# Optimization experiments

Measured on AMD Instinct MI355X. Metric: run time of the kernel, lower is better.

## Reference

```python
import jax, jax.numpy as jnp
import numpy as np

S, B, I, H = 512, 64, 1024, 1024


def setup_inputs() -> dict:
    key = jax.random.key(0)
    ks = jax.random.split(key, 17)
    sI = 1.0 / np.sqrt(I)
    sH = 1.0 / np.sqrt(H)
    d = {"x": jax.random.normal(ks[0], (S, B, I), dtype=jnp.float32)}
    names = ["i", "f", "c", "o"]
    for n, g in enumerate(names):
        d[f"w_x{g}"] = jax.random.uniform(ks[1 + 4 * n], (H, I), jnp.float32, -sI, sI)
        d[f"b_x{g}"] = jax.random.uniform(ks[2 + 4 * n], (H,), jnp.float32, -sI, sI)
        d[f"w_h{g}"] = jax.random.uniform(ks[3 + 4 * n], (H, H), jnp.float32, -sH, sH)
        d[f"b_h{g}"] = jax.random.uniform(ks[4 + 4 * n], (H,), jnp.float32, -sH, sH)
        d[f"b_{g}"] = jnp.zeros((H,), jnp.float32)
    return d


def reference(x, w_xi, b_xi, w_hi, b_hi, b_i,
              w_xf, b_xf, w_hf, b_hf, b_f,
              w_xc, b_xc, w_hc, b_hc, b_c,
              w_xo, b_xo, w_ho, b_ho, b_o):
    seq_len, batch, _ = x.shape
    hid = w_hi.shape[0]
    # Precompute all input-side projections in one big GEMM per gate: [S,B,H].
    # Fold the three bias vectors of each gate (b_x*, b_h*, b_*) in here; math
    # is identical to adding them per step.
    gx_i = jnp.einsum('sbi,hi->sbh', x, w_xi) + (b_xi + b_hi + b_i)
    gx_f = jnp.einsum('sbi,hi->sbh', x, w_xf) + (b_xf + b_hf + b_f)
    gx_c = jnp.einsum('sbi,hi->sbh', x, w_xc) + (b_xc + b_hc + b_c)
    gx_o = jnp.einsum('sbi,hi->sbh', x, w_xo) + (b_xo + b_ho + b_o)

    h0 = jnp.zeros((batch, hid), x.dtype)
    c0 = jnp.zeros((batch, hid), x.dtype)

    def step(carry, gx):
        h, c = carry
        xi, xf, xc, xo = gx
        i_t = jax.nn.sigmoid(xi + h @ w_hi.T)
        f_t = jax.nn.sigmoid(xf + h @ w_hf.T)
        g_t = jnp.tanh(xc + h @ w_hc.T)
        o_t = jax.nn.sigmoid(xo + h @ w_ho.T)
        c = f_t * c + i_t * g_t
        h = o_t * jnp.tanh(c)
        return (h, c), h

    (h, c), outputs = jax.lax.scan(step, (h0, c0), (gx_i, gx_f, gx_c, gx_o))
    return outputs, (h, c)
```

## Files before the change

kernel.cpp:

```cpp
#include <hip/hip_runtime.h>
#include <cstdint>
#include <cstddef>

#define S_LEN 512
#define NB    64
#define NI    1024
#define NH    1024
#define NR    4096
#define NGRP  4
#define WPG   64
#define BPG   16
#define HSLOT 33792
#define FLAGSTRIDE 16

typedef short bf16x8 __attribute__((ext_vector_type(8)));
typedef float f32x4  __attribute__((ext_vector_type(4)));

__device__ __forceinline__ short f2bf(float f) {
  uint32_t u = __float_as_uint(f);
  u += 0x7fff + ((u >> 16) & 1);
  return (short)(u >> 16);
}
__device__ __forceinline__ float bf2f(short s) {
  return __uint_as_float(((uint32_t)(uint16_t)s) << 16);
}
__device__ __forceinline__ void gload16(const void* g, void* l) {
  __builtin_amdgcn_global_load_lds((const __attribute__((address_space(1))) void*)g,
                                   (__attribute__((address_space(3))) void*)l, 16, 0, 0);
}
__device__ __forceinline__ float sigm(float x) { return 1.0f / (1.0f + __expf(-x)); }
__device__ __forceinline__ float tanh_fast(float x) {
  return 2.0f / (1.0f + __expf(-2.0f * x)) - 1.0f;
}

__device__ __forceinline__ void astore32(void* p, uint32_t v) {
  __hip_atomic_store((uint32_t*)p, v, __ATOMIC_RELAXED, __HIP_MEMORY_SCOPE_AGENT);
}
__device__ __forceinline__ void astore16(void* p, uint16_t v) {
  __hip_atomic_store((uint16_t*)p, v, __ATOMIC_RELAXED, __HIP_MEMORY_SCOPE_AGENT);
}
__device__ __forceinline__ uint32_t aload32(const void* p) {
  return __hip_atomic_load((const uint32_t*)p, __ATOMIC_RELAXED, __HIP_MEMORY_SCOPE_AGENT);
}


__global__ __launch_bounds__(256) void k_convert_x(const float* __restrict__ x,
                                                   short* __restrict__ xbf) {
  int tid = blockIdx.x * 256 + threadIdx.x;
  float4 v = ((const float4*)x)[tid];
  short4 o;
  o.x = f2bf(v.x); o.y = f2bf(v.y); o.z = f2bf(v.z); o.w = f2bf(v.w);
  ((short4*)xbf)[tid] = o;
}

struct WPtrs { const float *xi, *xf, *xc, *xo, *hi, *hf, *hc, *ho; };

__global__ __launch_bounds__(256) void k_pack_w(WPtrs w, short* __restrict__ wxcat,
                                                short* __restrict__ whcat) {
  int tid  = blockIdx.x * 256 + threadIdx.x;
  int flat = tid * 4;
  int r = flat >> 10, k = flat & 1023;
  int j = r >> 2, g = r & 3;
  const float* px = (g == 0) ? w.xi : (g == 1) ? w.xf : (g == 2) ? w.xc : w.xo;
  const float* ph = (g == 0) ? w.hi : (g == 1) ? w.hf : (g == 2) ? w.hc : w.ho;
  float4 vx = *(const float4*)(px + j * 1024 + k);
  float4 vh = *(const float4*)(ph + j * 1024 + k);
  short4 ox, oh;
  ox.x = f2bf(vx.x); ox.y = f2bf(vx.y); ox.z = f2bf(vx.z); ox.w = f2bf(vx.w);
  oh.x = f2bf(vh.x); oh.y = f2bf(vh.y); oh.z = f2bf(vh.z); oh.w = f2bf(vh.w);
  *(short4*)(wxcat + flat) = ox;
  *(short4*)(whcat + flat) = oh;
}

struct BPtrs { const float *xi,*hi,*i_, *xf,*hf,*f_, *xc,*hc,*c_, *xo,*ho,*o_; };

__global__ __launch_bounds__(256) void k_init(BPtrs p, float* __restrict__ bias,
                                              unsigned int* __restrict__ flags) {
  int tid = blockIdx.x * 256 + threadIdx.x;
  flags[tid] = 0;
  int j = tid >> 2, g = tid & 3;
  const float* bx = (g == 0) ? p.xi : (g == 1) ? p.xf : (g == 2) ? p.xc : p.xo;
  const float* bh = (g == 0) ? p.hi : (g == 1) ? p.hf : (g == 2) ? p.hc : p.ho;
  const float* bb = (g == 0) ? p.i_ : (g == 1) ? p.f_ : (g == 2) ? p.c_ : p.o_;
  bias[tid] = bx[j] + bh[j] + bb[j];
}


__global__ __launch_bounds__(256) void gemm_x(const short* __restrict__ xbf,
                                              const short* __restrict__ wx,
                                              const float* __restrict__ bias,
                                              short* __restrict__ gx) {
  __shared__ __align__(16) short As[2][4096];
  __shared__ __align__(16) short Bs[2][4096];

  const int tid = threadIdx.x, wave = tid >> 6, lane = tid & 63;
  const int m0 = blockIdx.x * 128, n0 = blockIdx.y * 128;
  const char* aB = (const char*)xbf + (size_t)m0 * 2048;
  const char* bB = (const char*)wx + (size_t)n0 * 2048;

  f32x4 acc[4][4] = {};

  auto stage = [&](int kt, int buf) {
#pragma unroll
    for (int s2 = 0; s2 < 2; ++s2) {
      int seg = wave * 2 + s2;
      int L   = seg * 1024 + lane * 16;
      int row = L >> 6;
      int cb  = L & 63;
      gload16(aB + (size_t)row * 2048 + kt * 64 + cb, (char*)&As[buf][0] + L);
      gload16(bB + (size_t)row * 2048 + kt * 64 + cb, (char*)&Bs[buf][0] + L);
    }
  };

  const int wm = wave >> 1, wn = wave & 1;
  auto compute = [&](int buf) {
    const char* Ab = (const char*)&As[buf][0];
    const char* Bb = (const char*)&Bs[buf][0];
    bf16x8 a[4], b[4];
#pragma unroll
    for (int f = 0; f < 4; ++f) {
      int ar = wm * 64 + f * 16 + (lane & 15);
      a[f] = *(const bf16x8*)(Ab + ar * 64 + (lane >> 4) * 16);
      int br = wn * 64 + f * 16 + (lane & 15);
      b[f] = *(const bf16x8*)(Bb + br * 64 + (lane >> 4) * 16);
    }
#pragma unroll
    for (int i = 0; i < 4; ++i)
#pragma unroll
      for (int j = 0; j < 4; ++j)
        acc[i][j] = __builtin_amdgcn_mfma_f32_16x16x32_bf16(a[i], b[j], acc[i][j], 0, 0, 0);
  };

  stage(0, 0);
  __syncthreads();
  int buf = 0;
  for (int kt = 0; kt < 32; ++kt) {
    if (kt < 31) stage(kt + 1, buf ^ 1);
    compute(buf);
    __syncthreads();
    buf ^= 1;
  }

  const int colL = lane & 15;
#pragma unroll
  for (int j = 0; j < 4; ++j) {
    int   n  = n0 + wn * 64 + j * 16 + colL;
    float bv = bias[n];
#pragma unroll
    for (int i = 0; i < 4; ++i) {
#pragma unroll
      for (int q = 0; q < 4; ++q) {
        int m = m0 + wm * 64 + i * 16 + (lane >> 4) * 4 + q;
        __builtin_nontemporal_store((short)f2bf(acc[i][j][q] + bv),
                                    &gx[(size_t)m * NR + n]);
      }
    }
  }
}

#define LDS_BYTES 131072

__global__ __launch_bounds__(256, 1) void lstm_persist(
    const short* __restrict__ gx,
    const short* __restrict__ wh,
    char* __restrict__ hb,
    unsigned int* __restrict__ flags,
    float* __restrict__ out) {
  extern __shared__ __align__(16) char lds[];
  char* WhC = lds;

  const int tid = threadIdx.x, wave = tid >> 6, lane = tid & 63;
  const int grp = blockIdx.x & 3;
  const int wq  = blockIdx.x >> 2;
  const int r0  = wq * 64;
  const int j0  = wq * 16;
  const char* whB = (const char*)(wh + (size_t)r0 * NH);
  char* hb_g = hb + (size_t)grp * S_LEN * HSLOT;
  unsigned int* flags_g = flags + grp * WPG * FLAGSTRIDE;

#pragma unroll
  for (int p = 0; p < 32; ++p) {
    int L = p * 4096 + tid * 16;
    int row = L >> 11, kb = L & 2047;
    gload16(whB + (size_t)row * 2048 + (kb ^ ((row & 7) << 4)), lds + L);
  }

  const int b_ln = lane & 15;
  const int jl   = wave * 4 + (lane >> 4);
  float c_reg = 0.f;

  const int aoff = (lane >> 5) * 512 + (lane & 15) * 32 + ((lane >> 4) & 1) * 16;
  const int br   = wave * 16 + (lane & 15);
  const int bswz = (br & 7) << 4;
  const int bcol = (lane >> 4) * 16;

  const unsigned int* fpoll = flags_g + lane * FLAGSTRIDE;

  const short* gx_me = gx + ((size_t)grp * BPG + b_ln) * NR + (j0 + jl) * 4;
  char* h_me = hb_g + wq * 512 + b_ln * 32 + jl * 2;
  float* out_me = out + (size_t)(grp * BPG + b_ln) * NH + j0 + jl;

  __syncthreads();

  short4 gx_cur = *(const short4*)(gx_me);
  short4 gx_nxt;

  for (int t = 0; t < S_LEN; ++t) {
    f32x4 acc0 = {}, acc1 = {};
    if (t) {
      const char* hs = hb_g + (size_t)(t - 1) * HSLOT + aoff;
      bf16x8 a[32];
#pragma unroll
      for (int ks = 0; ks < 32; ++ks)
        a[ks] = *(const bf16x8*)(hs + ks * 1024);
      {
        const int tp = (t + 1 < S_LEN) ? t + 1 : t;
        gx_nxt = *(const short4*)(gx_me + (size_t)tp * NB * NR);
      }
      __builtin_amdgcn_sched_barrier(0);
#pragma unroll
      for (int ks = 0; ks < 32; ++ks) {
        int wb = ks * 64 + bcol;
        bf16x8 w0 = *(const bf16x8*)(WhC + br * 2048 + (wb ^ bswz));
        if (ks & 1) acc1 = __builtin_amdgcn_mfma_f32_16x16x32_bf16(w0, a[ks], acc1, 0, 0, 0);
        else        acc0 = __builtin_amdgcn_mfma_f32_16x16x32_bf16(w0, a[ks], acc0, 0, 0, 0);
      }
    } else {
      gx_nxt = *(const short4*)(gx_me + (size_t)NB * NR);
    }

    f32x4 a0 = acc0 + acc1;
    float vi = a0[0] + bf2f(gx_cur.x);
    float vf = a0[1] + bf2f(gx_cur.y);
    float vg = a0[2] + bf2f(gx_cur.z);
    float vo = a0[3] + bf2f(gx_cur.w);
    float ig = sigm(vi), fg = sigm(vf), gg = tanh_fast(vg), og = sigm(vo);
    c_reg = fg * c_reg + ig * gg;
    float hn = og * tanh_fast(c_reg);

    if (t != S_LEN - 1)
      astore16(h_me + (size_t)t * HSLOT, (uint16_t)(uint16_t)f2bf(hn));
    out_me[(size_t)t * NB * NH] = hn;
    if (t == S_LEN - 1) {
      float* oh = out + (size_t)S_LEN * NB * NH;
      size_t ci = (size_t)(grp * BPG + b_ln) * NH + j0 + jl;
      oh[ci] = hn;
      oh[(size_t)NB * NH + ci] = c_reg;
    }

    if (t != S_LEN - 1) {
      __syncthreads();
      const unsigned want = (unsigned)(t + 1);
      if (tid == 0) astore32((void*)(flags_g + wq * FLAGSTRIDE), want);
      if (wave == 0) {
        uint32_t v = aload32(fpoll);
        while (!__all(v >= want)) {
          __builtin_amdgcn_s_sleep(1);
          v = aload32(fpoll);
        }
      }
      __syncthreads();
      gx_cur = gx_nxt;
    }
  }
}


extern "C" void kernel_launch(void* const* d_in, const int* in_sizes, int n_in,
                              void* d_out, int out_size, void* d_ws, size_t ws_size,
                              hipStream_t stream) {
  const float* x   = (const float*)d_in[0];
  const float* wxi = (const float*)d_in[1];
  const float* bxi = (const float*)d_in[2];
  const float* whi = (const float*)d_in[3];
  const float* bhi = (const float*)d_in[4];
  const float* bi  = (const float*)d_in[5];
  const float* wxf = (const float*)d_in[6];
  const float* bxf = (const float*)d_in[7];
  const float* whf = (const float*)d_in[8];
  const float* bhf = (const float*)d_in[9];
  const float* bf  = (const float*)d_in[10];
  const float* wxc = (const float*)d_in[11];
  const float* bxc = (const float*)d_in[12];
  const float* whc = (const float*)d_in[13];
  const float* bhc = (const float*)d_in[14];
  const float* bc  = (const float*)d_in[15];
  const float* wxo = (const float*)d_in[16];
  const float* bxo = (const float*)d_in[17];
  const float* who = (const float*)d_in[18];
  const float* bho = (const float*)d_in[19];
  const float* bo  = (const float*)d_in[20];

  char* ws = (char*)d_ws;
  const size_t SB = (size_t)S_LEN * NB;
  size_t off = 0;
  short* gxp   = (short*)(ws + off); off += SB * NR * 2;
  short* xbf   = (short*)(ws + off); off += SB * NI * 2;
  short* wxcat = (short*)(ws + off); off += (size_t)NR * NI * 2;
  short* whcat = (short*)(ws + off); off += (size_t)NR * NH * 2;
  float* bias  = (float*)(ws + off); off += NR * 4;
  unsigned int* flags = (unsigned int*)(ws + off); off += NGRP * WPG * FLAGSTRIDE * 4;
  (void)ws_size; (void)in_sizes; (void)n_in; (void)out_size;

  char* hb = (char*)xbf;

  float* out = (float*)d_out;

  (void)hipFuncSetAttribute((const void*)lstm_persist,
                            hipFuncAttributeMaxDynamicSharedMemorySize, LDS_BYTES);

  k_convert_x<<<(int)(SB * NI / 4 / 256), 256, 0, stream>>>(x, xbf);
  WPtrs wp = {wxi, wxf, wxc, wxo, whi, whf, whc, who};
  k_pack_w<<<(NR * NI / 4) / 256, 256, 0, stream>>>(wp, wxcat, whcat);
  BPtrs bp = {bxi, bhi, bi, bxf, bhf, bf, bxc, bhc, bc, bxo, bho, bo};
  k_init<<<NR / 256, 256, 0, stream>>>(bp, bias, flags);

  gemm_x<<<dim3(SB / 128, NR / 128), 256, 0, stream>>>(xbf, wxcat, bias, gxp);

  lstm_persist<<<NGRP * WPG, 256, LDS_BYTES, stream>>>(gxp, whcat, hb, flags, out);
}
```

Before: 2.246 ms.

## Fuse input projection GEMM into persistent LSTM kernel with lookahead pipeline

```diff
diff --git a/kernel.cpp b/kernel.cpp
--- a/kernel.cpp
+++ b/kernel.cpp
@@ -12,6 +12,7 @@
 #define BPG   16
 #define HSLOT 33792
 #define FLAGSTRIDE 16
+#define P_AHEAD 8
 
 typedef short bf16x8 __attribute__((ext_vector_type(8)));
 typedef float f32x4  __attribute__((ext_vector_type(4)));
@@ -85,84 +86,13 @@
   bias[tid] = bx[j] + bh[j] + bb[j];
 }
 
-
-__global__ __launch_bounds__(256) void gemm_x(const short* __restrict__ xbf,
-                                              const short* __restrict__ wx,
-                                              const float* __restrict__ bias,
-                                              short* __restrict__ gx) {
-  __shared__ __align__(16) short As[2][4096];
-  __shared__ __align__(16) short Bs[2][4096];
-
-  const int tid = threadIdx.x, wave = tid >> 6, lane = tid & 63;
-  const int m0 = blockIdx.x * 128, n0 = blockIdx.y * 128;
-  const char* aB = (const char*)xbf + (size_t)m0 * 2048;
-  const char* bB = (const char*)wx + (size_t)n0 * 2048;
-
-  f32x4 acc[4][4] = {};
-
-  auto stage = [&](int kt, int buf) {
-#pragma unroll
-    for (int s2 = 0; s2 < 2; ++s2) {
-      int seg = wave * 2 + s2;
-      int L   = seg * 1024 + lane * 16;
-      int row = L >> 6;
-      int cb  = L & 63;
-      gload16(aB + (size_t)row * 2048 + kt * 64 + cb, (char*)&As[buf][0] + L);
-      gload16(bB + (size_t)row * 2048 + kt * 64 + cb, (char*)&Bs[buf][0] + L);
-    }
-  };
-
-  const int wm = wave >> 1, wn = wave & 1;
-  auto compute = [&](int buf) {
-    const char* Ab = (const char*)&As[buf][0];
-    const char* Bb = (const char*)&Bs[buf][0];
-    bf16x8 a[4], b[4];
-#pragma unroll
-    for (int f = 0; f < 4; ++f) {
-      int ar = wm * 64 + f * 16 + (lane & 15);
-      a[f] = *(const bf16x8*)(Ab + ar * 64 + (lane >> 4) * 16);
-      int br = wn * 64 + f * 16 + (lane & 15);
-      b[f] = *(const bf16x8*)(Bb + br * 64 + (lane >> 4) * 16);
-    }
-#pragma unroll
-    for (int i = 0; i < 4; ++i)
-#pragma unroll
-      for (int j = 0; j < 4; ++j)
-        acc[i][j] = __builtin_amdgcn_mfma_f32_16x16x32_bf16(a[i], b[j], acc[i][j], 0, 0, 0);
-  };
-
-  stage(0, 0);
-  __syncthreads();
-  int buf = 0;
-  for (int kt = 0; kt < 32; ++kt) {
-    if (kt < 31) stage(kt + 1, buf ^ 1);
-    compute(buf);
-    __syncthreads();
-    buf ^= 1;
-  }
-
-  const int colL = lane & 15;
-#pragma unroll
-  for (int j = 0; j < 4; ++j) {
-    int   n  = n0 + wn * 64 + j * 16 + colL;
-    float bv = bias[n];
-#pragma unroll
-    for (int i = 0; i < 4; ++i) {
-#pragma unroll
-      for (int q = 0; q < 4; ++q) {
-        int m = m0 + wm * 64 + i * 16 + (lane >> 4) * 4 + q;
-        __builtin_nontemporal_store((short)f2bf(acc[i][j][q] + bv),
-                                    &gx[(size_t)m * NR + n]);
-      }
-    }
-  }
-}
-
 #define LDS_BYTES 131072
 
 __global__ __launch_bounds__(256, 1) void lstm_persist(
-    const short* __restrict__ gx,
+    const short* __restrict__ xbf,
+    const short* __restrict__ wx,
     const short* __restrict__ wh,
+    const float* __restrict__ bias,
     char* __restrict__ hb,
     unsigned int* __restrict__ flags,
     float* __restrict__ out) {
@@ -187,23 +117,48 @@
 
   const int b_ln = lane & 15;
   const int jl   = wave * 4 + (lane >> 4);
+  const int arow = wave * 16 + (lane & 15);
   float c_reg = 0.f;
 
+  bf16x8 wxr[32];
+  {
+    const short* wxp = wx + (size_t)(r0 + arow) * NI + (lane >> 4) * 8;
+#pragma unroll
+    for (int ks = 0; ks < 32; ++ks)
+      wxr[ks] = *(const bf16x8*)(wxp + ks * 32);
+  }
+
   const int aoff = (lane >> 5) * 512 + (lane & 15) * 32 + ((lane >> 4) & 1) * 16;
-  const int br   = wave * 16 + (lane & 15);
-  const int bswz = (br & 7) << 4;
+  const int bswz = (arow & 7) << 4;
   const int bcol = (lane >> 4) * 16;
+  const short* xme = xbf + ((size_t)grp * BPG + (lane & 15)) * NI + (lane >> 4) * 8;
+
+  const f32x4 bias_r = *(const f32x4*)(bias + (j0 + jl) * 4);
 
   const unsigned int* fpoll = flags_g + lane * FLAGSTRIDE;
-
-  const short* gx_me = gx + ((size_t)grp * BPG + b_ln) * NR + (j0 + jl) * 4;
-  char* h_me = hb_g + wq * 512 + b_ln * 32 + jl * 2;
+  char*  h_me   = hb_g + wq * 512 + b_ln * 32 + jl * 2;
   float* out_me = out + (size_t)(grp * BPG + b_ln) * NH + j0 + jl;
 
   __syncthreads();
 
-  short4 gx_cur = *(const short4*)(gx_me);
-  short4 gx_nxt;
+  uint2 gxr[P_AHEAD];
+#pragma unroll
+  for (int p = 0; p < P_AHEAD; ++p) {
+    const short* xs = xme + (size_t)p * NB * NI;
+    bf16x8 xb[32];
+#pragma unroll
+    for (int ks = 0; ks < 32; ++ks)
+      xb[ks] = *(const bf16x8*)(xs + ks * 32);
+    f32x4 g0 = {}, g1 = {};
+#pragma unroll
+    for (int ks = 0; ks < 32; ++ks) {
+      if (ks & 1) g1 = __builtin_amdgcn_mfma_f32_16x16x32_bf16(wxr[ks], xb[ks], g1, 0, 0, 0);
+      else        g0 = __builtin_amdgcn_mfma_f32_16x16x32_bf16(wxr[ks], xb[ks], g0, 0, 0, 0);
+    }
+    f32x4 gs = g0 + g1;
+    gxr[p].x = (uint32_t)(uint16_t)f2bf(gs[0]) | ((uint32_t)(uint16_t)f2bf(gs[1]) << 16);
+    gxr[p].y = (uint32_t)(uint16_t)f2bf(gs[2]) | ((uint32_t)(uint16_t)f2bf(gs[3]) << 16);
+  }
 
   for (int t = 0; t < S_LEN; ++t) {
     f32x4 acc0 = {}, acc1 = {};
@@ -213,33 +168,30 @@
 #pragma unroll
       for (int ks = 0; ks < 32; ++ks)
         a[ks] = *(const bf16x8*)(hs + ks * 1024);
-      {
-        const int tp = (t + 1 < S_LEN) ? t + 1 : t;
-        gx_nxt = *(const short4*)(gx_me + (size_t)tp * NB * NR);
-      }
       __builtin_amdgcn_sched_barrier(0);
 #pragma unroll
       for (int ks = 0; ks < 32; ++ks) {
         int wb = ks * 64 + bcol;
-        bf16x8 w0 = *(const bf16x8*)(WhC + br * 2048 + (wb ^ bswz));
+        bf16x8 w0 = *(const bf16x8*)(WhC + arow * 2048 + (wb ^ bswz));
         if (ks & 1) acc1 = __builtin_amdgcn_mfma_f32_16x16x32_bf16(w0, a[ks], acc1, 0, 0, 0);
         else        acc0 = __builtin_amdgcn_mfma_f32_16x16x32_bf16(w0, a[ks], acc0, 0, 0, 0);
       }
-    } else {
-      gx_nxt = *(const short4*)(gx_me + (size_t)NB * NR);
-    }
-
-    f32x4 a0 = acc0 + acc1;
-    float vi = a0[0] + bf2f(gx_cur.x);
-    float vf = a0[1] + bf2f(gx_cur.y);
-    float vg = a0[2] + bf2f(gx_cur.z);
-    float vo = a0[3] + bf2f(gx_cur.w);
+    }
+
+    f32x4 ah = acc0 + acc1;
+    float vi = ah[0] + bf2f((short)(gxr[0].x & 0xffff))  + bias_r[0];
+    float vf = ah[1] + bf2f((short)(gxr[0].x >> 16))     + bias_r[1];
+    float vg = ah[2] + bf2f((short)(gxr[0].y & 0xffff))  + bias_r[2];
+    float vo = ah[3] + bf2f((short)(gxr[0].y >> 16))     + bias_r[3];
     float ig = sigm(vi), fg = sigm(vf), gg = tanh_fast(vg), og = sigm(vo);
     c_reg = fg * c_reg + ig * gg;
     float hn = og * tanh_fast(c_reg);
 
+#pragma unroll
+    for (int i = 0; i < P_AHEAD - 1; ++i) gxr[i] = gxr[i + 1];
+
     if (t != S_LEN - 1)
-      astore16(h_me + (size_t)t * HSLOT, (uint16_t)(uint16_t)f2bf(hn));
+      astore16(h_me + (size_t)t * HSLOT, (uint16_t)f2bf(hn));
     out_me[(size_t)t * NB * NH] = hn;
     if (t == S_LEN - 1) {
       float* oh = out + (size_t)S_LEN * NB * NH;
@@ -252,6 +204,24 @@
       __syncthreads();
       const unsigned want = (unsigned)(t + 1);
       if (tid == 0) astore32((void*)(flags_g + wq * FLAGSTRIDE), want);
+
+      if (t + P_AHEAD < S_LEN) {
+        const short* xs = xme + (size_t)(t + P_AHEAD) * NB * NI;
+        bf16x8 xb[32];
+#pragma unroll
+        for (int ks = 0; ks < 32; ++ks)
+          xb[ks] = *(const bf16x8*)(xs + ks * 32);
+        f32x4 g0 = {}, g1 = {};
+#pragma unroll
+        for (int ks = 0; ks < 32; ++ks) {
+          if (ks & 1) g1 = __builtin_amdgcn_mfma_f32_16x16x32_bf16(wxr[ks], xb[ks], g1, 0, 0, 0);
+          else        g0 = __builtin_amdgcn_mfma_f32_16x16x32_bf16(wxr[ks], xb[ks], g0, 0, 0, 0);
+        }
+        f32x4 gs = g0 + g1;
+        gxr[P_AHEAD - 1].x = (uint32_t)(uint16_t)f2bf(gs[0]) | ((uint32_t)(uint16_t)f2bf(gs[1]) << 16);
+        gxr[P_AHEAD - 1].y = (uint32_t)(uint16_t)f2bf(gs[2]) | ((uint32_t)(uint16_t)f2bf(gs[3]) << 16);
+      }
+
       if (wave == 0) {
         uint32_t v = aload32(fpoll);
         while (!__all(v >= want)) {
@@ -260,7 +230,6 @@
         }
       }
       __syncthreads();
-      gx_cur = gx_nxt;
     }
   }
 }
@@ -294,15 +263,13 @@
   char* ws = (char*)d_ws;
   const size_t SB = (size_t)S_LEN * NB;
   size_t off = 0;
-  short* gxp   = (short*)(ws + off); off += SB * NR * 2;
   short* xbf   = (short*)(ws + off); off += SB * NI * 2;
   short* wxcat = (short*)(ws + off); off += (size_t)NR * NI * 2;
   short* whcat = (short*)(ws + off); off += (size_t)NR * NH * 2;
   float* bias  = (float*)(ws + off); off += NR * 4;
   unsigned int* flags = (unsigned int*)(ws + off); off += NGRP * WPG * FLAGSTRIDE * 4;
+  char* hb     = ws + off; off += (size_t)NGRP * S_LEN * HSLOT;
   (void)ws_size; (void)in_sizes; (void)n_in; (void)out_size;
-
-  char* hb = (char*)xbf;
 
   float* out = (float*)d_out;
 
@@ -315,7 +282,6 @@
   BPtrs bp = {bxi, bhi, bi, bxf, bhf, bf, bxc, bhc, bc, bxo, bho, bo};
   k_init<<<NR / 256, 256, 0, stream>>>(bp, bias, flags);
 
-  gemm_x<<<dim3(SB / 128, NR / 128), 256, 0, stream>>>(xbf, wxcat, bias, gxp);
-
-  lstm_persist<<<NGRP * WPG, 256, LDS_BYTES, stream>>>(gxp, whcat, hb, flags, out);
-}
+  lstm_persist<<<NGRP * WPG, 256, LDS_BYTES, stream>>>(xbf, wxcat, whcat, bias,
+                                                       hb, flags, out);
+}
```

New measurement: 4.104 ms. 1.83x slower.
